# Performance work log

Measured on AMD Instinct MI355X. Metric: run time of the kernel, lower is better.

The kernel has to match this reference:

```python
import jax, jax.numpy as jnp
import numpy as np

B, S, D, H, W = 2, 2048, 1024, 16, 16  # batch, seq, embed, heads, window
HD = D // H
DFF = 4 * D
EPS = 1e-5


def _ln(x, g, b):
    m = jnp.mean(x, axis=-1, keepdims=True)
    v = jnp.mean(jnp.square(x - m), axis=-1, keepdims=True)
    return (x - m) * jax.lax.rsqrt(v + EPS) * g + b


def setup_inputs() -> dict:
    key = jax.random.key(0)
    ks = jax.random.split(key, 12)
    s = 0.02
    return {
        "x": jax.random.normal(ks[0], (B, S, D), jnp.float32),
        "ln1_g": jnp.ones((D,), jnp.float32),
        "ln1_b": jnp.zeros((D,), jnp.float32),
        "in_proj_w": jax.random.normal(ks[1], (3 * D, D), jnp.float32) * s,
        "in_proj_b": jnp.zeros((3 * D,), jnp.float32),
        "out_proj_w": jax.random.normal(ks[2], (D, D), jnp.float32) * s,
        "out_proj_b": jnp.zeros((D,), jnp.float32),
        "ln2_g": jnp.ones((D,), jnp.float32),
        "ln2_b": jnp.zeros((D,), jnp.float32),
        "mlp_w1": jax.random.normal(ks[3], (DFF, D), jnp.float32) * s,
        "mlp_b1": jnp.zeros((DFF,), jnp.float32),
        "mlp_w2": jax.random.normal(ks[4], (D, DFF), jnp.float32) * s,
        "mlp_b2": jnp.zeros((D,), jnp.float32),
    }


def reference(x, ln1_g, ln1_b, in_proj_w, in_proj_b, out_proj_w, out_proj_b,
              ln2_g, ln2_b, mlp_w1, mlp_b1, mlp_w2, mlp_b2):
    h = _ln(x, ln1_g, ln1_b)
    qkv = h @ in_proj_w.T + in_proj_b  # [B,S,3D]
    q, k, v = jnp.split(qkv, 3, axis=-1)
    q = q.reshape(B, S, H, HD)
    k = k.reshape(B, S, H, HD)
    v = v.reshape(B, S, H, HD)
    scores = jnp.einsum("bqhd,bkhd->bhqk", q, k) / jnp.sqrt(jnp.float32(HD))
    idx = jnp.arange(S)
    dlt = idx[:, None] - idx[None, :]
    allowed = (dlt >= 0) & (dlt < W)  # causal sliding window, width W
    scores = jnp.where(allowed, scores, -jnp.inf)
    attn = jax.nn.softmax(scores, axis=-1)
    o = jnp.einsum("bhqk,bkhd->bqhd", attn, v).reshape(B, S, D)
    o = o @ out_proj_w.T + out_proj_b
    x = x + o  # residual 1
    xn = _ln(x, ln2_g, ln2_b)
    mlp = jax.nn.gelu(xn @ mlp_w1.T + mlp_b1) @ mlp_w2.T + mlp_b2
    return x + mlp
```

## Files before the change

### kernel.cpp

```cpp
#include <hip/hip_runtime.h>
#include <hip/hip_bf16.h>
#include <cmath>

typedef __bf16 bf16;
typedef __bf16 bf16x4 __attribute__((ext_vector_type(4)));
typedef __bf16 bf16x8 __attribute__((ext_vector_type(8)));
typedef float f32x4 __attribute__((ext_vector_type(4)));

#define BB 2
#define SS 2048
#define DD 1024
#define HH 16
#define WW 16
#define HDD 64
#define DFFD 4096
#define NTOK (BB*SS)

__device__ __forceinline__ float gelu_f(float x) {
    const float k = 1.5957691216057308f;
    float u = k * (x + 0.044715f * x * x * x);
    return x / (1.0f + __expf(-u));
}

__device__ __forceinline__ void glds16(const bf16* g, const bf16* l) {
    __builtin_amdgcn_global_load_lds(
        (const __attribute__((address_space(1))) void*)(uintptr_t)(const void*)g,
        (__attribute__((address_space(3))) void*)(unsigned)(uintptr_t)(const void*)l,
        16, 0, 0);
}

__global__ __launch_bounds__(256) void conv_kernel(
    const float* __restrict__ src, bf16* __restrict__ dst, int n8)
{
    int i = blockIdx.x * 256 + threadIdx.x;
    if (i >= n8) return;
    f32x4 a = *(const f32x4*)(src + (size_t)i * 8);
    f32x4 b = *(const f32x4*)(src + (size_t)i * 8 + 4);
    bf16x8 v;
#pragma unroll
    for (int j = 0; j < 4; j++) { v[j] = (bf16)a[j]; v[4 + j] = (bf16)b[j]; }
    *(bf16x8*)(dst + (size_t)i * 8) = v;
}

__global__ __launch_bounds__(256) void ln_kernel(
    const float* __restrict__ x, const float* __restrict__ g, const float* __restrict__ b,
    bf16* __restrict__ out)
{
    const int row = blockIdx.x, t = threadIdx.x;
    f32x4 v = *(const f32x4*)(x + (size_t)row * DD + t * 4);
    float s  = v[0] + v[1] + v[2] + v[3];
    float s2 = v[0]*v[0] + v[1]*v[1] + v[2]*v[2] + v[3]*v[3];
#pragma unroll
    for (int off = 32; off >= 1; off >>= 1) {
        s  += __shfl_xor(s,  off, 64);
        s2 += __shfl_xor(s2, off, 64);
    }
    __shared__ float red[8];
    const int wave = t >> 6;
    if ((t & 63) == 0) { red[wave] = s; red[4 + wave] = s2; }
    __syncthreads();
    float ts  = red[0] + red[1] + red[2] + red[3];
    float ts2 = red[4] + red[5] + red[6] + red[7];
    float mean = ts * (1.0f / DD);
    float var  = ts2 * (1.0f / DD) - mean * mean;
    float rstd = rsqrtf(var + 1e-5f);
    f32x4 gv = *(const f32x4*)(g + t * 4);
    f32x4 bv = *(const f32x4*)(b + t * 4);
    bf16x4 o;
#pragma unroll
    for (int i = 0; i < 4; i++) o[i] = (bf16)((v[i] - mean) * rstd * gv[i] + bv[i]);
    *(bf16x4*)(out + (size_t)row * DD + t * 4) = o;
}

template<int ACT, int RESID, int OUTF32>
__global__ __launch_bounds__(512, 2) void gemm_8p(
    const bf16* __restrict__ A, const bf16* __restrict__ Bw,
    const float* __restrict__ bias,
    void* __restrict__ Cout, int N, int K)
{
    __shared__ __align__(16) bf16 ring[4][16384];
    const int t512 = threadIdx.x;
    const int lane = t512 & 63, w = t512 >> 6;
    const int quad = lane >> 4, l16 = lane & 15;
    const int wm = (w >> 2) * 128;
    const int wn = (w & 3) * 64;

    const int nb  = gridDim.x * gridDim.y;
    const int bid = blockIdx.y * gridDim.x + blockIdx.x;
    const int cpx = nb >> 3;
    const int swz = (bid & 7) * cpx + (bid >> 3);
    const int m0 = (swz / gridDim.x) * 256;
    const int n0 = (swz % gridDim.x) * 256;

    int k_lo = 0, k_hi = K;
    if (RESID == 3) { const int ks = K / gridDim.z; k_lo = blockIdx.z * ks; k_hi = k_lo + ks; }
    const int NK = (k_hi - k_lo) >> 5;

    const int srow = t512 >> 2;
    auto stageA = [&](int u) {
        const int k0 = k_lo + (u << 5);
        const bf16* dst = ring[u & 3] + w * 512;
#pragma unroll
        for (int ra = 0; ra < 2; ra++) {
            const int row = ra * 128 + srow;
            const int q = (t512 & 3) ^ (row & 3);
            glds16(A + (size_t)(m0 + row) * K + k0 + q * 8, dst + ra * 4096);
        }
    };
    auto stageB = [&](int u) {
        const int k0 = k_lo + (u << 5);
        const bf16* dst = ring[u & 3] + 8192 + w * 512;
#pragma unroll
        for (int ra = 0; ra < 2; ra++) {
            const int row = ra * 128 + srow;
            const int q = (t512 & 3) ^ (row & 3);
            glds16(Bw + (size_t)(n0 + row) * K + k0 + q * 8, dst + ra * 4096);
        }
    };

    const f32x4 zero = {0.f, 0.f, 0.f, 0.f};
    f32x4 acc[8][4];
#pragma unroll
    for (int i = 0; i < 8; i++)
#pragma unroll
        for (int j = 0; j < 4; j++) acc[i][j] = zero;

    for (int u = 0; u < 3 && u < NK; ++u) { stageA(u); stageB(u); }

    const int aswz = (l16 & 3);
    for (int t = 0; t < NK; ++t) {
        if (t < NK - 2)       asm volatile("s_waitcnt vmcnt(8)" ::: "memory");
        else if (t == NK - 2) asm volatile("s_waitcnt vmcnt(4)" ::: "memory");
        else                  asm volatile("s_waitcnt vmcnt(0)" ::: "memory");
        __builtin_amdgcn_s_barrier();
        const bf16* Ab = ring[t & 3];
        const bf16* Bb = Ab + 8192;
        bf16x8 af[4], bfr[4];
#pragma unroll
        for (int i = 0; i < 4; i++) {
            const int row = wm + i * 16 + l16;
            af[i] = *(const bf16x8*)(Ab + row * 32 + ((quad ^ aswz) * 8));
        }
#pragma unroll
        for (int j = 0; j < 4; j++) {
            const int row = wn + j * 16 + l16;
            bfr[j] = *(const bf16x8*)(Bb + row * 32 + ((quad ^ aswz) * 8));
        }
        if (t + 3 < NK) stageA(t + 3);
        asm volatile("s_waitcnt lgkmcnt(0)" ::: "memory");
        __builtin_amdgcn_sched_barrier(0);
        __builtin_amdgcn_s_setprio(1);
#pragma unroll
        for (int i = 0; i < 4; i++)
#pragma unroll
            for (int j = 0; j < 4; j++)
                acc[i][j] = __builtin_amdgcn_mfma_f32_16x16x32_bf16(af[i], bfr[j], acc[i][j], 0, 0, 0);
        __builtin_amdgcn_s_setprio(0);
        __builtin_amdgcn_s_barrier();
#pragma unroll
        for (int i = 0; i < 4; i++) {
            const int row = wm + 64 + i * 16 + l16;
            af[i] = *(const bf16x8*)(Ab + row * 32 + ((quad ^ aswz) * 8));
        }
        if (t + 3 < NK) stageB(t + 3);
        asm volatile("s_waitcnt lgkmcnt(0)" ::: "memory");
        __builtin_amdgcn_sched_barrier(0);
        __builtin_amdgcn_s_setprio(1);
#pragma unroll
        for (int i = 0; i < 4; i++)
#pragma unroll
            for (int j = 0; j < 4; j++)
                acc[4 + i][j] = __builtin_amdgcn_mfma_f32_16x16x32_bf16(af[i], bfr[j], acc[4 + i][j], 0, 0, 0);
        __builtin_amdgcn_s_setprio(0);
    }

#pragma unroll
    for (int i = 0; i < 8; i++) {
#pragma unroll
        for (int j = 0; j < 4; j++) {
            const int col = n0 + wn + j * 16 + l16;
            float bv = bias[col];
            if (RESID == 3 && blockIdx.z != 0) bv = 0.0f;
#pragma unroll
            for (int r = 0; r < 4; r++) {
                const int row = m0 + wm + i * 16 + quad * 4 + r;
                float val = acc[i][j][r] + bv;
                if (ACT == 1) val = gelu_f(val);
                size_t idx = (size_t)row * N + col;
                if (RESID == 3) {
                    unsafeAtomicAdd(&((float*)Cout)[idx], val);
                } else if (OUTF32) {
                    ((float*)Cout)[idx] = val;
                } else {
                    ((bf16*)Cout)[idx] = (bf16)val;
                }
            }
        }
    }
}

template<int TM, int ACT, int RESID, int OUTF32>
__global__ __launch_bounds__(256) void gemm_glds(
    const bf16* __restrict__ A, const bf16* __restrict__ Bw,
    const float* __restrict__ bias,
    const float* resid, void* __restrict__ Cout, int N, int K)
{
    constexpr int MI = 4;
    constexpr int NJ = (TM == 128) ? 4 : 2;
    __shared__ __align__(16) bf16 As[2 * TM * 32];
    __shared__ __align__(16) bf16 Bs[2 * 128 * 32];
    const int t = threadIdx.x;
    const int m0 = blockIdx.y * TM, n0 = blockIdx.x * 128;
    const int lane = t & 63, w = t >> 6;
    const int wm = (TM == 128) ? (w & 1) * 64 : 0;
    const int wn = (TM == 128) ? (w >> 1) * 64 : w * 32;
    const int quad = lane >> 4, l16 = lane & 15;
    const int srow = t >> 2, scol = (t & 3) * 8;

    const bf16* Ag = A  + (size_t)(m0 + srow) * K + scol;
    const bf16* Bg = Bw + (size_t)(n0 + srow) * K + scol;

    auto stage = [&](int buf, int k0) {
        const bf16* AsW = As + buf * (TM * 32) + w * 512;
        const bf16* BsW = Bs + buf * (128 * 32) + w * 512;
        glds16(Ag + k0, AsW);
        if (TM == 128) glds16(Ag + (size_t)64 * K + k0, AsW + 2048);
        glds16(Bg + k0, BsW);
        glds16(Bg + (size_t)64 * K + k0, BsW + 2048);
    };

    const f32x4 zero = {0.f, 0.f, 0.f, 0.f};
    f32x4 acc[MI][NJ];
#pragma unroll
    for (int i = 0; i < MI; i++)
#pragma unroll
        for (int j = 0; j < NJ; j++) acc[i][j] = zero;

    const int nsteps = K >> 5;
    stage(0, 0);
    __syncthreads();

    for (int step = 0; step < nsteps; ++step) {
        const int cur = step & 1;
        if (step + 1 < nsteps)
            stage(cur ^ 1, (step + 1) << 5);
        const bf16* Ab = As + cur * (TM * 32);
        const bf16* Bb = Bs + cur * (128 * 32);
        bf16x8 af[MI], bfr[NJ];
#pragma unroll
        for (int i = 0; i < MI; i++)
            af[i] = *(const bf16x8*)(Ab + (wm + i * 16 + l16) * 32 + quad * 8);
#pragma unroll
        for (int j = 0; j < NJ; j++)
            bfr[j] = *(const bf16x8*)(Bb + (wn + j * 16 + l16) * 32 + quad * 8);
#pragma unroll
        for (int i = 0; i < MI; i++)
#pragma unroll
            for (int j = 0; j < NJ; j++)
                acc[i][j] = __builtin_amdgcn_mfma_f32_16x16x32_bf16(af[i], bfr[j], acc[i][j], 0, 0, 0);
        __syncthreads();
    }

#pragma unroll
    for (int i = 0; i < MI; i++) {
#pragma unroll
        for (int j = 0; j < NJ; j++) {
            int col = n0 + wn + j * 16 + l16;
            float bv = bias[col];
#pragma unroll
            for (int r = 0; r < 4; r++) {
                int row = m0 + wm + i * 16 + quad * 4 + r;
                float val = acc[i][j][r] + bv;
                if (ACT == 1) val = gelu_f(val);
                size_t idx = (size_t)row * N + col;
                if (RESID == 2) val += resid[idx];
                if (OUTF32) ((float*)Cout)[idx] = val;
                else        ((bf16*)Cout)[idx] = (bf16)val;
            }
        }
    }
}

__global__ __launch_bounds__(256) void attn_kernel(
    const bf16* __restrict__ qkv, bf16* __restrict__ o)
{
    __shared__ __align__(16) bf16 Vlds[4][32 * 64];
    __shared__ __align__(16) bf16 Plds[4][16 * 32];
    const int t = threadIdx.x;
    const int w = t >> 6, lane = t & 63;
    const int quad = lane >> 4, l16 = lane & 15;
    const int gw = blockIdx.x * 4 + w;
    const int qb = gw & 127;
    const int h  = (gw >> 7) & (HH - 1);
    const int b  = gw >> 11;
    const int q0 = qb << 4;
    const size_t rs = 3 * DD;
    const bf16* Qb = qkv + (size_t)b * SS * rs + h * HDD;
    const bf16* Kb = Qb + DD;
    const bf16* Vb = Qb + 2 * DD;
    bf16* Vw = Vlds[w];
    bf16* Pw = Plds[w];

    {
        const int sub = lane >> 3;
        const int dc  = (lane & 7) * 8;
#pragma unroll
        for (int c = 0; c < 4; c++) {
            int key = q0 - 16 + c * 8 + sub;
            if (key < 0) key = 0;
            glds16(Vb + (size_t)key * rs + dc, Vw + c * 512);
        }
    }

    const int qrow = q0 + l16;
    int kr0 = q0 - 16 + l16; if (kr0 < 0) kr0 = 0;
    bf16x8 qf0  = *(const bf16x8*)(Qb + (size_t)qrow * rs + quad * 8);
    bf16x8 qf1  = *(const bf16x8*)(Qb + (size_t)qrow * rs + 32 + quad * 8);
    bf16x8 kf0a = *(const bf16x8*)(Kb + (size_t)kr0  * rs + quad * 8);
    bf16x8 kf0b = *(const bf16x8*)(Kb + (size_t)kr0  * rs + 32 + quad * 8);
    bf16x8 kf1a = *(const bf16x8*)(Kb + (size_t)qrow * rs + quad * 8);
    bf16x8 kf1b = *(const bf16x8*)(Kb + (size_t)qrow * rs + 32 + quad * 8);

    const f32x4 zero = {0.f, 0.f, 0.f, 0.f};
    f32x4 acc0 = __builtin_amdgcn_mfma_f32_16x16x32_bf16(qf0, kf0a, zero, 0, 0, 0);
    acc0 = __builtin_amdgcn_mfma_f32_16x16x32_bf16(qf1, kf0b, acc0, 0, 0, 0);
    f32x4 acc1 = __builtin_amdgcn_mfma_f32_16x16x32_bf16(qf0, kf1a, zero, 0, 0, 0);
    acc1 = __builtin_amdgcn_mfma_f32_16x16x32_bf16(qf1, kf1b, acc1, 0, 0, 0);

    float rl[4];
#pragma unroll
    for (int r = 0; r < 4; r++) {
        const int row = quad * 4 + r;
        float s0 = (l16 > row && q0 - 16 + l16 >= 0) ? acc0[r] * 0.125f : -1e30f;
        float s1 = (l16 <= row)                      ? acc1[r] * 0.125f : -1e30f;
        float m = fmaxf(s0, s1);
        m = fmaxf(m, __shfl_xor(m, 1, 64));
        m = fmaxf(m, __shfl_xor(m, 2, 64));
        m = fmaxf(m, __shfl_xor(m, 4, 64));
        m = fmaxf(m, __shfl_xor(m, 8, 64));
        float e0 = __expf(s0 - m), e1 = __expf(s1 - m);
        float sum = e0 + e1;
        sum += __shfl_xor(sum, 1, 64);
        sum += __shfl_xor(sum, 2, 64);
        sum += __shfl_xor(sum, 4, 64);
        sum += __shfl_xor(sum, 8, 64);
        rl[r] = 1.0f / sum;
        Pw[row * 32 + l16]      = (bf16)e0;
        Pw[row * 32 + 16 + l16] = (bf16)e1;
    }

    asm volatile("s_waitcnt vmcnt(0)" ::: "memory");
    bf16x8 pf = *(const bf16x8*)(Pw + l16 * 32 + quad * 8);
#pragma unroll
    for (int dt = 0; dt < 4; dt++) {
        bf16x8 vf;
#pragma unroll
        for (int jj = 0; jj < 8; jj++)
            vf[jj] = Vw[(quad * 8 + jj) * 64 + dt * 16 + l16];
        f32x4 ov = __builtin_amdgcn_mfma_f32_16x16x32_bf16(pf, vf, zero, 0, 0, 0);
#pragma unroll
        for (int r = 0; r < 4; r++) {
            const int row = quad * 4 + r;
            o[(size_t)(b * SS + q0 + row) * DD + h * HDD + dt * 16 + l16] =
                (bf16)(ov[r] * rl[r]);
        }
    }
}

extern "C" void kernel_launch(void* const* d_in, const int* in_sizes, int n_in,
                              void* d_out, int out_size, void* d_ws, size_t ws_size,
                              hipStream_t stream)
{
    (void)in_sizes; (void)n_in; (void)out_size; (void)ws_size;
    const float* x    = (const float*)d_in[0];
    const float* ln1g = (const float*)d_in[1];
    const float* ln1b = (const float*)d_in[2];
    const float* Wqkv = (const float*)d_in[3];
    const float* bqkv = (const float*)d_in[4];
    const float* Wout = (const float*)d_in[5];
    const float* bout = (const float*)d_in[6];
    const float* ln2g = (const float*)d_in[7];
    const float* ln2b = (const float*)d_in[8];
    const float* W1   = (const float*)d_in[9];
    const float* b1   = (const float*)d_in[10];
    const float* W2   = (const float*)d_in[11];
    const float* b2   = (const float*)d_in[12];

    const size_t MB = (size_t)1 << 20;
    char* ws = (char*)d_ws;
    bf16* wqkv_bf = (bf16*)(ws);
    bf16* wout_bf = (bf16*)(ws + 6 * MB);
    bf16* w1_bf   = (bf16*)(ws);
    bf16* w2_bf   = (bf16*)(ws + 8 * MB);
    bf16* qkv     = (bf16*)(ws + 16 * MB);
    bf16* h1      = (bf16*)(ws + 16 * MB);
    bf16* hbuf    = (bf16*)(ws + 48 * MB);
    float* x1     = (float*)d_out;

    const dim3 blk(256);
    const dim3 blk512(512);

    conv_kernel<<<(3 * DD * DD / 8) / 256, blk, 0, stream>>>(Wqkv, wqkv_bf, 3 * DD * DD / 8);
    conv_kernel<<<(DD * DD / 8) / 256, blk, 0, stream>>>(Wout, wout_bf, DD * DD / 8);
    ln_kernel<<<NTOK, blk, 0, stream>>>(x, ln1g, ln1b, hbuf);
    gemm_8p<0, 0, 0><<<dim3(12, 16), blk512, 0, stream>>>(
        hbuf, wqkv_bf, bqkv, qkv, 3 * DD, DD);
    attn_kernel<<<BB * HH * (SS / 16) / 4, blk, 0, stream>>>(qkv, hbuf);
    gemm_glds<64, 0, 2, 1><<<dim3(8, 64), blk, 0, stream>>>(
        hbuf, wout_bf, bout, x, x1, DD, DD);

    conv_kernel<<<(DFFD * DD / 8) / 256, blk, 0, stream>>>(W1, w1_bf, DFFD * DD / 8);
    conv_kernel<<<(DFFD * DD / 8) / 256, blk, 0, stream>>>(W2, w2_bf, DFFD * DD / 8);
    ln_kernel<<<NTOK, blk, 0, stream>>>(x1, ln2g, ln2b, hbuf);
    gemm_8p<1, 0, 0><<<dim3(16, 16), blk512, 0, stream>>>(
        hbuf, w1_bf, b1, h1, DFFD, DD);
    gemm_8p<0, 3, 1><<<dim3(4, 16, 4), blk512, 0, stream>>>(
        h1, w2_bf, b2, x1, DD, DFFD);
}
```

Before: 318.0 us.

## Move MLP down-projection split-K to 128-tile gemm and change LDS swizzle

Changes the LDS XOR swizzle in the 8-phase GEMM from row&3 to (row>>1)&3 on both the staging and read sides, aiming to cut bank conflicts on the fragment reads. Also moves the split-K fp32-atomic down-projection from the 256x256 8-phase kernel (4-way split, 256 blocks) to the double-buffered 128x128 gemm_glds kernel with a 2-way split (512 blocks). The smaller tiles give more blocks and fewer atomic partial sums, in exchange for a shallower pipeline and less data reuse per block.

```diff
diff --git a/kernel.cpp b/kernel.cpp
--- a/kernel.cpp
+++ b/kernel.cpp
@@ -72,7 +72,7 @@
     *(bf16x4*)(out + (size_t)row * DD + t * 4) = o;
 }
 
-template<int ACT, int RESID, int OUTF32>
+template<int ACT>
 __global__ __launch_bounds__(512, 2) void gemm_8p(
     const bf16* __restrict__ A, const bf16* __restrict__ Bw,
     const float* __restrict__ bias,
@@ -92,29 +92,26 @@
     const int m0 = (swz / gridDim.x) * 256;
     const int n0 = (swz % gridDim.x) * 256;
 
-    int k_lo = 0, k_hi = K;
-    if (RESID == 3) { const int ks = K / gridDim.z; k_lo = blockIdx.z * ks; k_hi = k_lo + ks; }
-    const int NK = (k_hi - k_lo) >> 5;
+    const int NK = K >> 5;
 
     const int srow = t512 >> 2;
+    const int qsw  = (t512 & 3) ^ ((srow >> 1) & 3);
     auto stageA = [&](int u) {
-        const int k0 = k_lo + (u << 5);
+        const int k0 = (u << 5);
         const bf16* dst = ring[u & 3] + w * 512;
 #pragma unroll
         for (int ra = 0; ra < 2; ra++) {
             const int row = ra * 128 + srow;
-            const int q = (t512 & 3) ^ (row & 3);
-            glds16(A + (size_t)(m0 + row) * K + k0 + q * 8, dst + ra * 4096);
+            glds16(A + (size_t)(m0 + row) * K + k0 + qsw * 8, dst + ra * 4096);
         }
     };
     auto stageB = [&](int u) {
-        const int k0 = k_lo + (u << 5);
+        const int k0 = (u << 5);
         const bf16* dst = ring[u & 3] + 8192 + w * 512;
 #pragma unroll
         for (int ra = 0; ra < 2; ra++) {
             const int row = ra * 128 + srow;
-            const int q = (t512 & 3) ^ (row & 3);
-            glds16(Bw + (size_t)(n0 + row) * K + k0 + q * 8, dst + ra * 4096);
+            glds16(Bw + (size_t)(n0 + row) * K + k0 + qsw * 8, dst + ra * 4096);
         }
     };
 
@@ -127,7 +124,7 @@
 
     for (int u = 0; u < 3 && u < NK; ++u) { stageA(u); stageB(u); }
 
-    const int aswz = (l16 & 3);
+    const int rsl = (quad ^ ((l16 >> 1) & 3)) * 8;
     for (int t = 0; t < NK; ++t) {
         if (t < NK - 2)       asm volatile("s_waitcnt vmcnt(8)" ::: "memory");
         else if (t == NK - 2) asm volatile("s_waitcnt vmcnt(4)" ::: "memory");
@@ -137,15 +134,11 @@
         const bf16* Bb = Ab + 8192;
         bf16x8 af[4], bfr[4];
 #pragma unroll
-        for (int i = 0; i < 4; i++) {
-            const int row = wm + i * 16 + l16;
-            af[i] = *(const bf16x8*)(Ab + row * 32 + ((quad ^ aswz) * 8));
-        }
-#pragma unroll
-        for (int j = 0; j < 4; j++) {
-            const int row = wn + j * 16 + l16;
-            bfr[j] = *(const bf16x8*)(Bb + row * 32 + ((quad ^ aswz) * 8));
-        }
+        for (int i = 0; i < 4; i++)
+            af[i] = *(const bf16x8*)(Ab + (wm + i * 16 + l16) * 32 + rsl);
+#pragma unroll
+        for (int j = 0; j < 4; j++)
+            bfr[j] = *(const bf16x8*)(Bb + (wn + j * 16 + l16) * 32 + rsl);
         if (t + 3 < NK) stageA(t + 3);
         asm volatile("s_waitcnt lgkmcnt(0)" ::: "memory");
         __builtin_amdgcn_sched_barrier(0);
@@ -158,10 +151,8 @@
         __builtin_amdgcn_s_setprio(0);
         __builtin_amdgcn_s_barrier();
 #pragma unroll
-        for (int i = 0; i < 4; i++) {
-            const int row = wm + 64 + i * 16 + l16;
-            af[i] = *(const bf16x8*)(Ab + row * 32 + ((quad ^ aswz) * 8));
-        }
+        for (int i = 0; i < 4; i++)
+            af[i] = *(const bf16x8*)(Ab + (wm + 64 + i * 16 + l16) * 32 + rsl);
         if (t + 3 < NK) stageB(t + 3);
         asm volatile("s_waitcnt lgkmcnt(0)" ::: "memory");
         __builtin_amdgcn_sched_barrier(0);
@@ -180,20 +171,12 @@
         for (int j = 0; j < 4; j++) {
             const int col = n0 + wn + j * 16 + l16;
             float bv = bias[col];
-            if (RESID == 3 && blockIdx.z != 0) bv = 0.0f;
 #pragma unroll
             for (int r = 0; r < 4; r++) {
                 const int row = m0 + wm + i * 16 + quad * 4 + r;
                 float val = acc[i][j][r] + bv;
                 if (ACT == 1) val = gelu_f(val);
-                size_t idx = (size_t)row * N + col;
-                if (RESID == 3) {
-                    unsafeAtomicAdd(&((float*)Cout)[idx], val);
-                } else if (OUTF32) {
-                    ((float*)Cout)[idx] = val;
-                } else {
-                    ((bf16*)Cout)[idx] = (bf16)val;
-                }
+                ((bf16*)Cout)[(size_t)row * N + col] = (bf16)val;
             }
         }
     }
@@ -220,6 +203,13 @@
     const bf16* Ag = A  + (size_t)(m0 + srow) * K + scol;
     const bf16* Bg = Bw + (size_t)(n0 + srow) * K + scol;
 
+    int k_lo = 0, k_hi = K;
+    if (RESID == 3) {
+        const int ks = K / gridDim.z;
+        k_lo = blockIdx.z * ks;
+        k_hi = k_lo + ks;
+    }
+
     auto stage = [&](int buf, int k0) {
         const bf16* AsW = As + buf * (TM * 32) + w * 512;
         const bf16* BsW = Bs + buf * (128 * 32) + w * 512;
@@ -236,14 +226,14 @@
 #pragma unroll
         for (int j = 0; j < NJ; j++) acc[i][j] = zero;
 
-    const int nsteps = K >> 5;
-    stage(0, 0);
+    const int nsteps = (k_hi - k_lo) >> 5;
+    stage(0, k_lo);
     __syncthreads();
 
     for (int step = 0; step < nsteps; ++step) {
         const int cur = step & 1;
         if (step + 1 < nsteps)
-            stage(cur ^ 1, (step + 1) << 5);
+            stage(cur ^ 1, k_lo + ((step + 1) << 5));
         const bf16* Ab = As + cur * (TM * 32);
         const bf16* Bb = Bs + cur * (128 * 32);
         bf16x8 af[MI], bfr[NJ];
@@ -267,6 +257,7 @@
         for (int j = 0; j < NJ; j++) {
             int col = n0 + wn + j * 16 + l16;
             float bv = bias[col];
+            if (RESID == 3 && blockIdx.z != 0) bv = 0.0f;
 #pragma unroll
             for (int r = 0; r < 4; r++) {
                 int row = m0 + wm + i * 16 + quad * 4 + r;
@@ -274,8 +265,13 @@
                 if (ACT == 1) val = gelu_f(val);
                 size_t idx = (size_t)row * N + col;
                 if (RESID == 2) val += resid[idx];
-                if (OUTF32) ((float*)Cout)[idx] = val;
-                else        ((bf16*)Cout)[idx] = (bf16)val;
+                if (RESID == 3) {
+                    unsafeAtomicAdd(&((float*)Cout)[idx], val);
+                } else if (OUTF32) {
+                    ((float*)Cout)[idx] = val;
+                } else {
+                    ((bf16*)Cout)[idx] = (bf16)val;
+                }
             }
         }
     }
@@ -403,7 +399,7 @@
     conv_kernel<<<(3 * DD * DD / 8) / 256, blk, 0, stream>>>(Wqkv, wqkv_bf, 3 * DD * DD / 8);
     conv_kernel<<<(DD * DD / 8) / 256, blk, 0, stream>>>(Wout, wout_bf, DD * DD / 8);
     ln_kernel<<<NTOK, blk, 0, stream>>>(x, ln1g, ln1b, hbuf);
-    gemm_8p<0, 0, 0><<<dim3(12, 16), blk512, 0, stream>>>(
+    gemm_8p<0><<<dim3(12, 16), blk512, 0, stream>>>(
         hbuf, wqkv_bf, bqkv, qkv, 3 * DD, DD);
     attn_kernel<<<BB * HH * (SS / 16) / 4, blk, 0, stream>>>(qkv, hbuf);
     gemm_glds<64, 0, 2, 1><<<dim3(8, 64), blk, 0, stream>>>(
@@ -412,8 +408,8 @@
     conv_kernel<<<(DFFD * DD / 8) / 256, blk, 0, stream>>>(W1, w1_bf, DFFD * DD / 8);
     conv_kernel<<<(DFFD * DD / 8) / 256, blk, 0, stream>>>(W2, w2_bf, DFFD * DD / 8);
     ln_kernel<<<NTOK, blk, 0, stream>>>(x1, ln2g, ln2b, hbuf);
-    gemm_8p<1, 0, 0><<<dim3(16, 16), blk512, 0, stream>>>(
+    gemm_8p<1><<<dim3(16, 16), blk512, 0, stream>>>(
         hbuf, w1_bf, b1, h1, DFFD, DD);
-    gemm_8p<0, 3, 1><<<dim3(4, 16, 4), blk512, 0, stream>>>(
-        h1, w2_bf, b2, x1, DD, DFFD);
-}
+    gemm_glds<128, 0, 3, 1><<<dim3(8, 32, 2), blk, 0, stream>>>(
+        h1, w2_bf, b2, nullptr, x1, DD, DFFD);
+}
```

Result: faster. 305.4 us (-4.0%).
